# Kernel tuning notes

Hardware: AMD Instinct MI355X
Metric: run time of the kernel (lower is better)

Reference implementation:

```python
import jax, jax.numpy as jnp
import numpy as np

TEMPERATURE = 0.1
EPS = 1e-8


def _hann(T, dtype):
    # torch.hann_window default: periodic=True -> 0.5*(1-cos(2*pi*n/T))
    return 0.5 * (1.0 - jnp.cos(2.0 * jnp.pi * jnp.arange(T, dtype=dtype) / T))


def _per_traj_stats(trajectories):
    # trajectories: [B, T, 4] = (phi1, v1, phi2, v2)
    B, T, _ = trajectories.shape
    v = trajectories[:, :, 1::2]                      # [B, T, 2] voltages
    v_mean = v.mean(axis=1)                           # [B, 2]
    w = _hann(T, trajectories.dtype)[None, :, None]
    fft = jnp.fft.rfft(v * w, axis=1)                 # [B, T//2+1, 2]
    psd = (jnp.abs(fft) ** 2)[:, : T // 10, :]        # keep low-frequency bins
    psd = psd.reshape(B, -1)                          # [B, 2*(T//10)] (flatten, C-order like torch)
    phase = trajectories[:, :, 0::2]                  # [B, T, 2]
    delta = jnp.diff(phase, axis=1)
    winding = jnp.abs(jnp.round(delta.sum(axis=1) / (2.0 * jnp.pi)))  # [B, 2]
    return v_mean, psd, winding


def _kinematic_similarity(trajectories):
    # Vectorized equivalent of the original O(B^2) python loop (i < j, symmetrized, zero diag)
    v_mean, psd, winding = _per_traj_stats(trajectories)
    v_dist = jnp.linalg.norm(v_mean[:, None, :] - v_mean[None, :, :], axis=-1)  # [B, B]
    v_sim = jnp.exp(-v_dist / 0.5)
    n2 = jnp.sum(psd * psd, axis=1)                   # [B]
    gram = psd @ psd.T                                # [B, B]
    d2 = jnp.maximum(n2[:, None] + n2[None, :] - 2.0 * gram, 0.0)
    psd_dist = jnp.sqrt(d2)
    psd_norm = jnp.sqrt(n2)
    # denominator uses ||psd_i|| of the row index (matches loop where i < j)
    psd_sim = jnp.exp(-psd_dist / (psd_norm[:, None] + EPS))
    wind_sim = jnp.all(winding[:, None, :] == winding[None, :, :], axis=-1).astype(psd.dtype)
    total = 0.4 * v_sim + 0.4 * psd_sim + 0.2 * wind_sim
    upper = jnp.triu(total, k=1)                      # only i<j computed in the loop
    return upper + upper.T                            # symmetric, zero diagonal


def reference(features, labels, trajectories, param_scales):
    B = features.shape[0]
    # F.normalize(dim=1), eps=1e-12
    norm = jnp.maximum(jnp.linalg.norm(features, axis=1, keepdims=True), 1e-12)
    f = features / norm
    param_diff = jnp.abs(labels[:, None, :] - labels[None, :, :]) / param_scales
    param_dist = jnp.linalg.norm(param_diff, axis=2)  # [B, B]
    kin_sim = jax.lax.stop_gradient(_kinematic_similarity(trajectories))  # no_grad in torch
    mask_pos_weight = jnp.exp(-param_dist / 0.1) * kin_sim
    sim = (f @ f.T) / TEMPERATURE
    exp_sim = jnp.exp(sim)
    exp_sim = jnp.where(jnp.eye(B, dtype=bool), 0.0, exp_sim)
    pos_weighted = (exp_sim * mask_pos_weight).sum(axis=1)
    denom = exp_sim.sum(axis=1)
    loss = -jnp.log((pos_weighted + EPS) / (denom + EPS))
    return loss.mean()


def setup_inputs() -> dict:
    key = jax.random.key(0)
    k1, k2, k3 = jax.random.split(key, 3)
    B, D, T, P = 1024, 256, 8192, 3
    features = jax.random.normal(k1, (B, D), dtype=jnp.float32)
    labels = jax.random.uniform(k2, (B, P), dtype=jnp.float32)
    trajectories = jax.random.normal(k3, (B, T, 4), dtype=jnp.float32)
    param_scales = jnp.ones((1,), dtype=jnp.float32)
    return {"features": features, "labels": labels, "trajectories": trajectories, "param_scales": param_scales}
```

## Files before the change

### kernel.cpp

```cpp
#include <hip/hip_runtime.h>
#include <hip/hip_bf16.h>

#define B_SZ 1024
#define T_LEN 8192
#define NBINS 819
#define PSD_LDA 1664
#define PI_F 3.14159265358979323846f

typedef __attribute__((ext_vector_type(8))) short bf16x8;
typedef __attribute__((ext_vector_type(4))) float f32x4;

__device__ constexpr float W32C[32] = {
  1.0f, 0.980785280f, 0.923879533f, 0.831469612f, 0.707106781f, 0.555570233f,
  0.382683432f, 0.195090322f, 0.0f, -0.195090322f, -0.382683432f, -0.555570233f,
  -0.707106781f, -0.831469612f, -0.923879533f, -0.980785280f, -1.0f,
  -0.980785280f, -0.923879533f, -0.831469612f, -0.707106781f, -0.555570233f,
  -0.382683432f, -0.195090322f, 0.0f, 0.195090322f, 0.382683432f, 0.555570233f,
  0.707106781f, 0.831469612f, 0.923879533f, 0.980785280f};
__device__ constexpr float W32S[32] = {
  0.0f, -0.195090322f, -0.382683432f, -0.555570233f, -0.707106781f,
  -0.831469612f, -0.923879533f, -0.980785280f, -1.0f, -0.980785280f,
  -0.923879533f, -0.831469612f, -0.707106781f, -0.555570233f, -0.382683432f,
  -0.195090322f, 0.0f, 0.195090322f, 0.382683432f, 0.555570233f, 0.707106781f,
  0.831469612f, 0.923879533f, 0.980785280f, 1.0f, 0.980785280f, 0.923879533f,
  0.831469612f, 0.707106781f, 0.555570233f, 0.382683432f, 0.195090322f};
__device__ constexpr float E8C[8] = {
  1.0f, 0.707106781f, 0.0f, -0.707106781f, -1.0f, -0.707106781f, 0.0f, 0.707106781f};
__device__ constexpr float E8S[8] = {
  0.0f, 0.707106781f, 1.0f, 0.707106781f, 0.0f, -0.707106781f, -1.0f, -0.707106781f};

__device__ __forceinline__ unsigned short bfb(float x) {
  __hip_bfloat16 h = __float2bfloat16(x);
  return *(unsigned short*)&h;
}
__device__ __forceinline__ float bff(unsigned short u) {
  union { unsigned u; float f; } v; v.u = ((unsigned)u) << 16; return v.f;
}
__device__ __forceinline__ unsigned cvtpk(float r, float i) {
  unsigned out;
  asm("v_cvt_pk_bf16_f32 %0, %1, %2" : "=v"(out) : "v"(r), "v"(i));
  return out;
}
union U8 { bf16x8 v; unsigned u[4]; };

#define WIDX(k0, b, c) ((k0) * 288 + 9 * (b) + (c))

template<int K, int LDA>
__device__ __forceinline__ void gram_body(
    const __hip_bfloat16* __restrict__ A, float* __restrict__ C,
    int i0, int j0, int tid, void* ldsraw) {
  __hip_bfloat16 (*lds)[64][64] = (__hip_bfloat16 (*)[64][64])ldsraw;
  const int lane = tid & 63;
  const int wave = tid >> 6;
  const int wm = wave >> 1, wn = wave & 1;

  f32x4 acc[2][2] = {};

  for (int k0 = 0; k0 < K; k0 += 64) {
    #pragma unroll
    for (int r = 0; r < 2; ++r) {
      int e   = tid + 256 * r;
      int row = e >> 3;
      int cb  = e & 7;
      int scb = cb ^ (row & 7);
      const __hip_bfloat16* srcA = A + (size_t)(i0 + row) * LDA + k0 + scb * 8;
      const __hip_bfloat16* srcB = A + (size_t)(j0 + row) * LDA + k0 + scb * 8;
      __builtin_amdgcn_global_load_lds(
          (const __attribute__((address_space(1))) void*)srcA,
          (__attribute__((address_space(3))) void*)(&lds[0][0][0] + e * 8),
          16, 0, 0);
      __builtin_amdgcn_global_load_lds(
          (const __attribute__((address_space(1))) void*)srcB,
          (__attribute__((address_space(3))) void*)(&lds[1][0][0] + e * 8),
          16, 0, 0);
    }
    __syncthreads();

    #pragma unroll
    for (int ks = 0; ks < 2; ++ks) {
      bf16x8 afr[2], bfr[2];
      #pragma unroll
      for (int m = 0; m < 2; ++m) {
        int row = wm * 32 + m * 16 + (lane & 15);
        int cidx = ks * 4 + (lane >> 4);
        int cc  = cidx ^ (row & 7);
        afr[m] = *(const bf16x8*)(&lds[0][row][cc * 8]);
      }
      #pragma unroll
      for (int n = 0; n < 2; ++n) {
        int row = wn * 32 + n * 16 + (lane & 15);
        int cidx = ks * 4 + (lane >> 4);
        int cc  = cidx ^ (row & 7);
        bfr[n] = *(const bf16x8*)(&lds[1][row][cc * 8]);
      }
      #pragma unroll
      for (int m = 0; m < 2; ++m)
        #pragma unroll
        for (int n = 0; n < 2; ++n)
          acc[m][n] = __builtin_amdgcn_mfma_f32_16x16x32_bf16(
              afr[m], bfr[n], acc[m][n], 0, 0, 0);
    }
    __syncthreads();
  }

  #pragma unroll
  for (int m = 0; m < 2; ++m)
    #pragma unroll
    for (int n = 0; n < 2; ++n)
      #pragma unroll
      for (int r = 0; r < 4; ++r) {
        int row = i0 + wm * 32 + m * 16 + (lane >> 4) * 4 + r;
        int col = j0 + wn * 32 + n * 16 + (lane & 15);
        C[(size_t)row * B_SZ + col] = acc[m][n][r];
      }
}

__global__ __launch_bounds__(256) void normalize_kernel(
    const float* __restrict__ f, __hip_bfloat16* __restrict__ fn) {
  int i = blockIdx.x;
  int t = threadIdx.x;
  float v = f[(size_t)i * 256 + t];
  float s = v * v;
  #pragma unroll
  for (int o = 32; o; o >>= 1) s += __shfl_down(s, o);
  __shared__ float buf[4];
  if ((t & 63) == 0) buf[t >> 6] = s;
  __syncthreads();
  float norm = sqrtf(buf[0] + buf[1] + buf[2] + buf[3]);
  norm = fmaxf(norm, 1e-12f);
  fn[(size_t)i * 256 + t] = __float2bfloat16(v / norm);
}

__global__ __launch_bounds__(256) void traj_featgram_kernel(
    const float* __restrict__ trajf,
    __hip_bfloat16* __restrict__ psd,
    float2* __restrict__ vmean,
    float2* __restrict__ wind,
    const __hip_bfloat16* __restrict__ f_n,
    float* __restrict__ S) {
  __shared__ __align__(16) unsigned z2w[9216];
  __shared__ float rsum[2][4];
  __shared__ float phb[4];

  const int tid = threadIdx.x;

  if (blockIdx.x >= B_SZ) {
    const int e  = blockIdx.x - B_SZ;
    gram_body<256, 256>(f_n, S, (e >> 4) * 64, (e & 15) * 64, tid, (void*)z2w);
    return;
  }

  const int w   = tid >> 6;
  const int l   = tid & 63;
  const int g   = l >> 4;
  const int lc  = l & 15;
  const float* rowf = trajf + (size_t)blockIdx.x * T_LEN * 4;

  if (tid == 0) {
    phb[0] = rowf[0]; phb[1] = rowf[2];
    phb[2] = rowf[(size_t)4 * (T_LEN - 1)];
    phb[3] = rowf[(size_t)4 * (T_LEN - 1) + 2];
  }

  bf16x8 Ac[2], As[2], Asn[2];
  #pragma unroll
  for (int mt = 0; mt < 2; ++mt) {
    const int m = mt * 16 + lc;
    #pragma unroll
    for (int j = 0; j < 8; ++j) {
      const int idx = (m * (g * 8 + j)) & 31;
      unsigned short uc = bfb(W32C[idx]);
      unsigned short us = bfb(W32S[idx]);
      Ac[mt][j]  = (short)uc;
      As[mt][j]  = (short)us;
      Asn[mt][j] = (short)(us ^ 0x8000);
    }
  }

  float vs0 = 0.f, vs1 = 0.f;
  const f32x4 az = {0.f, 0.f, 0.f, 0.f};

  #pragma unroll
  for (int nt = 0; nt < 4; ++nt) {
    const int n = w * 64 + nt * 16 + lc;
    float yr[8], yw[8];
    #pragma unroll
    for (int j = 0; j < 8; ++j) {
      const size_t t = (size_t)(g * 8 + j) * 256 + n;
      yr[j] = rowf[4 * t + 1];
      yw[j] = rowf[4 * t + 3];
    }
    #pragma unroll
    for (int j = 0; j < 8; ++j) { vs0 += yr[j]; vs1 += yw[j]; }
    float s0, c0;
    __sincosf(2.0f * PI_F * ((float)n / 8192.0f + (float)g * 0.25f), &s0, &c0);
    U8 xrb, xib;
    #pragma unroll
    for (int j2 = 0; j2 < 4; ++j2) {
      float w0 = 0.5f - 0.5f * (c0 * W32C[2*j2]   + s0 * W32S[2*j2]);
      float w1 = 0.5f - 0.5f * (c0 * W32C[2*j2+1] + s0 * W32S[2*j2+1]);
      xrb.u[j2] = cvtpk(yr[2*j2] * w0, yr[2*j2+1] * w1);
      xib.u[j2] = cvtpk(yw[2*j2] * w0, yw[2*j2+1] * w1);
    }
    const int bw = 9 * (n >> 3) + (n & 7);
    float ss, cs;
    __sincosf(-2.0f * PI_F * (float)n / 8192.0f, &ss, &cs);
    #pragma unroll
    for (int mt = 0; mt < 2; ++mt) {
      f32x4 ar = __builtin_amdgcn_mfma_f32_16x16x32_bf16(Asn[mt], xib.v, az, 0, 0, 0);
      ar = __builtin_amdgcn_mfma_f32_16x16x32_bf16(Ac[mt], xrb.v, ar, 0, 0, 0);
      f32x4 ai = __builtin_amdgcn_mfma_f32_16x16x32_bf16(Ac[mt], xib.v, az, 0, 0, 0);
      ai = __builtin_amdgcn_mfma_f32_16x16x32_bf16(As[mt], xrb.v, ai, 0, 0, 0);
      float sb, cb;
      __sincosf(-2.0f * PI_F * (float)n * (float)(mt * 16 + g * 4) / 8192.0f, &sb, &cb);
      #pragma unroll
      for (int r = 0; r < 4; ++r) {
        float xr_ = ar[r] * cb - ai[r] * sb;
        float xi_ = ar[r] * sb + ai[r] * cb;
        const int k0 = mt * 16 + g * 4 + r;
        z2w[k0 * 288 + bw] = cvtpk(xr_, xi_);
        float nc = cb * cs - sb * ss; sb = cb * ss + sb * cs; cb = nc;
      }
    }
  }
  __syncthreads();

  unsigned x2_0[2][4], x2_1[2][4], x2_2[2][4], x2_3[2][4];
  #pragma unroll
  for (int nt = 0; nt < 4; ++nt) {
    const int n2 = w * 64 + nt * 16 + lc;
    const int k0 = n2 >> 3, cc = n2 & 7;
    U8 xrb, xib;
    #pragma unroll
    for (int j2 = 0; j2 < 4; ++j2) {
      unsigned p0 = z2w[WIDX(k0, g * 8 + 2*j2,     cc)];
      unsigned p1 = z2w[WIDX(k0, g * 8 + 2*j2 + 1, cc)];
      xrb.u[j2] = (p0 & 0xffffu) | (p1 << 16);
      xib.u[j2] = (p0 >> 16) | (p1 & 0xffff0000u);
    }
    #pragma unroll
    for (int mt = 0; mt < 2; ++mt) {
      f32x4 ar = __builtin_amdgcn_mfma_f32_16x16x32_bf16(Asn[mt], xib.v, az, 0, 0, 0);
      ar = __builtin_amdgcn_mfma_f32_16x16x32_bf16(Ac[mt], xrb.v, ar, 0, 0, 0);
      f32x4 ai = __builtin_amdgcn_mfma_f32_16x16x32_bf16(Ac[mt], xib.v, az, 0, 0, 0);
      ai = __builtin_amdgcn_mfma_f32_16x16x32_bf16(As[mt], xrb.v, ai, 0, 0, 0);
      float sb, cb, ss, cs;
      const float cf = (float)cc;
      __sincosf(-2.0f * PI_F * cf * (float)(mt * 16 + g * 4) / 256.0f, &sb, &cb);
      __sincosf(-2.0f * PI_F * cf / 256.0f, &ss, &cs);
      #pragma unroll
      for (int r = 0; r < 4; ++r) {
        float xr_ = ar[r] * cb - ai[r] * sb;
        float xi_ = ar[r] * sb + ai[r] * cb;
        unsigned pk = cvtpk(xr_, xi_);
        if (nt == 0) x2_0[mt][r] = pk;
        else if (nt == 1) x2_1[mt][r] = pk;
        else if (nt == 2) x2_2[mt][r] = pk;
        else x2_3[mt][r] = pk;
        float nc = cb * cs - sb * ss; sb = cb * ss + sb * cs; cb = nc;
      }
    }
  }
  __syncthreads();

  #pragma unroll
  for (int nt = 0; nt < 4; ++nt) {
    const int n2 = w * 64 + nt * 16 + lc;
    const int k0 = n2 >> 3, cc = n2 & 7;
    #pragma unroll
    for (int mt = 0; mt < 2; ++mt)
      #pragma unroll
      for (int r = 0; r < 4; ++r) {
        const int p = (mt * 16 + g * 4 + r) * 32 + k0;
        unsigned pk = (nt == 0) ? x2_0[mt][r] : (nt == 1) ? x2_1[mt][r]
                    : (nt == 2) ? x2_2[mt][r] : x2_3[mt][r];
        z2w[(p << 3) + (cc ^ ((p >> 2) & 7))] = pk;
      }
  }
  __syncthreads();

  float z0r[4], z0i[4], z7r[4], z7i[4];
  #pragma unroll
  for (int q = 0; q < 4; ++q) {
    const int p = q * 256 + tid;
    float s0r = 0.f, s0i = 0.f, s7r = 0.f, s7i = 0.f;
    #pragma unroll
    for (int c2 = 0; c2 < 8; ++c2) {
      unsigned pw = z2w[(p << 3) + (c2 ^ ((p >> 2) & 7))];
      float vr = bff((unsigned short)(pw & 0xffff));
      float vi = bff((unsigned short)(pw >> 16));
      s0r += vr; s0i += vi;
      s7r += vr * E8C[c2] - vi * E8S[c2];
      s7i += vr * E8S[c2] + vi * E8C[c2];
    }
    z0r[q] = s0r; z0i[q] = s0i; z7r[q] = s7r; z7i[q] = s7i;
  }
  __syncthreads();
  float2* zf = (float2*)z2w;
  #pragma unroll
  for (int q = 0; q < 4; ++q) {
    const int p = q * 256 + tid;
    zf[p]        = make_float2(z0r[q], z0i[q]);
    zf[1024 + p] = make_float2(z7r[q], z7i[q]);
  }
  __syncthreads();

  for (int k = tid; k < PSD_LDA / 2; k += 256) {
    if (k < NBINS) {
      float2 Zk = zf[k];
      float2 Zn = (k == 0) ? zf[0] : zf[2048 - k];
      float fxr = 0.5f * (Zk.x + Zn.x);
      float fxi = 0.5f * (Zk.y - Zn.y);
      float fyr = 0.5f * (Zk.y + Zn.y);
      float fyi = 0.5f * (Zn.x - Zk.x);
      psd[(size_t)blockIdx.x * PSD_LDA + 2*k]     = __float2bfloat16(fxr*fxr + fxi*fxi);
      psd[(size_t)blockIdx.x * PSD_LDA + 2*k + 1] = __float2bfloat16(fyr*fyr + fyi*fyi);
    } else {
      psd[(size_t)blockIdx.x * PSD_LDA + 2*k]     = __float2bfloat16(0.0f);
      psd[(size_t)blockIdx.x * PSD_LDA + 2*k + 1] = __float2bfloat16(0.0f);
    }
  }

  #pragma unroll
  for (int o = 32; o; o >>= 1) {
    vs0 += __shfl_down(vs0, o);
    vs1 += __shfl_down(vs1, o);
  }
  if ((tid & 63) == 0) { rsum[0][tid >> 6] = vs0; rsum[1][tid >> 6] = vs1; }
  __syncthreads();
  if (tid == 0) {
    float s0 = rsum[0][0] + rsum[0][1] + rsum[0][2] + rsum[0][3];
    float s1v = rsum[1][0] + rsum[1][1] + rsum[1][2] + rsum[1][3];
    vmean[blockIdx.x] = make_float2(s0 / (float)T_LEN, s1v / (float)T_LEN);
    const float inv2pi = 0.15915494309189535f;
    wind[blockIdx.x] = make_float2(fabsf(rintf((phb[2] - phb[0]) * inv2pi)),
                                   fabsf(rintf((phb[3] - phb[1]) * inv2pi)));
  }
}

template<int K, int LDA, int KOFF>
__global__ __launch_bounds__(256) void gram_mfma_kernel(
    const __hip_bfloat16* __restrict__ A, float* __restrict__ C) {
  __shared__ __align__(16) __hip_bfloat16 lds[2][64][64];
  gram_body<K, LDA>(A + (size_t)blockIdx.z * KOFF,
                    C + (size_t)blockIdx.z * B_SZ * B_SZ,
                    blockIdx.y * 64, blockIdx.x * 64, threadIdx.x, (void*)lds);
}

__global__ __launch_bounds__(256) void loss_rows_kernel(
    const float* __restrict__ S,
    const float* __restrict__ G,
    const float* __restrict__ labels,
    const float* __restrict__ scales,
    const float2* __restrict__ vmean,
    const float2* __restrict__ wind,
    float* __restrict__ row_loss) {
  const int i = blockIdx.x;
  const int tid = threadIdx.x;
  const float* G2 = G + (size_t)B_SZ * B_SZ;
  const float inv_scale = 1.0f / scales[0];
  const float l0 = labels[i*3+0], l1 = labels[i*3+1], l2 = labels[i*3+2];
  const float2 vmi = vmean[i];
  const float2 wi  = wind[i];
  const float n2i  = G[(size_t)i * B_SZ + i] + G2[(size_t)i * B_SZ + i];
  const float normi = sqrtf(n2i);

  float posw = 0.f, den = 0.f;
  for (int j = tid; j < B_SZ; j += 256) {
    if (j == i) continue;
    float e = __expf(S[(size_t)i * B_SZ + j] * 10.0f);
    den += e;

    float d0 = (labels[j*3+0] - l0) * inv_scale;
    float d1 = (labels[j*3+1] - l1) * inv_scale;
    float d2v = (labels[j*3+2] - l2) * inv_scale;
    float pd = sqrtf(d0*d0 + d1*d1 + d2v*d2v);
    float pw = __expf(-pd * 10.0f);

    float2 vmj = vmean[j];
    float dvx = vmi.x - vmj.x, dvy = vmi.y - vmj.y;
    float v_sim = __expf(-sqrtf(dvx*dvx + dvy*dvy) * 2.0f);

    float n2j = G[(size_t)j * B_SZ + j] + G2[(size_t)j * B_SZ + j];
    float gg  = G[(size_t)i * B_SZ + j] + G2[(size_t)i * B_SZ + j];
    float dd  = fmaxf(n2i + n2j - 2.0f * gg, 0.0f);
    float psd_dist = sqrtf(dd);
    float norma = (i < j) ? normi : sqrtf(n2j);
    float psd_sim = __expf(-psd_dist / (norma + 1e-8f));

    float2 wj = wind[j];
    float w_sim = (wi.x == wj.x && wi.y == wj.y) ? 1.0f : 0.0f;

    float kin = 0.4f * v_sim + 0.4f * psd_sim + 0.2f * w_sim;
    posw += e * pw * kin;
  }

  #pragma unroll
  for (int o = 32; o; o >>= 1) {
    posw += __shfl_down(posw, o);
    den  += __shfl_down(den, o);
  }
  __shared__ float bp[4], bd[4];
  if ((tid & 63) == 0) { bp[tid >> 6] = posw; bd[tid >> 6] = den; }
  __syncthreads();
  if (tid == 0) {
    float P = bp[0] + bp[1] + bp[2] + bp[3];
    float D = bd[0] + bd[1] + bd[2] + bd[3];
    row_loss[i] = -logf((P + 1e-8f) / (D + 1e-8f));
  }
}

__global__ __launch_bounds__(256) void reduce_mean_kernel(
    const float* __restrict__ row_loss, float* __restrict__ out) {
  int tid = threadIdx.x;
  float s = 0.f;
  for (int i = tid; i < B_SZ; i += 256) s += row_loss[i];
  #pragma unroll
  for (int o = 32; o; o >>= 1) s += __shfl_down(s, o);
  __shared__ float buf[4];
  if ((tid & 63) == 0) buf[tid >> 6] = s;
  __syncthreads();
  if (tid == 0) out[0] = (buf[0] + buf[1] + buf[2] + buf[3]) / (float)B_SZ;
}

extern "C" void kernel_launch(void* const* d_in, const int* in_sizes, int n_in,
                              void* d_out, int out_size, void* d_ws, size_t ws_size,
                              hipStream_t stream) {
  const float* features = (const float*)d_in[0];
  const float* labels   = (const float*)d_in[1];
  const float* traj     = (const float*)d_in[2];
  const float* scales   = (const float*)d_in[3];

  char* ws = (char*)d_ws;
  __hip_bfloat16* f_n = (__hip_bfloat16*)ws;
  __hip_bfloat16* psd = (__hip_bfloat16*)(ws + (size_t)B_SZ*256*2);
  float* G = (float*)(ws + (size_t)B_SZ*256*2 + (size_t)B_SZ*PSD_LDA*2);
  float* S = G + 2 * (size_t)B_SZ * B_SZ;
  float2* vmean = (float2*)(S + (size_t)B_SZ * B_SZ);
  float2* wind  = vmean + B_SZ;
  float* row_loss = (float*)(wind + B_SZ);

  normalize_kernel<<<B_SZ, 256, 0, stream>>>(features, f_n);
  traj_featgram_kernel<<<B_SZ + 256, 256, 0, stream>>>(
      traj, psd, vmean, wind, f_n, S);

  dim3 gridPsd(16, 16, 2);
  gram_mfma_kernel<832, PSD_LDA, 832><<<gridPsd, 256, 0, stream>>>(psd, G);

  loss_rows_kernel<<<B_SZ, 256, 0, stream>>>(S, G, labels, scales, vmean, wind, row_loss);
  reduce_mean_kernel<<<1, 256, 0, stream>>>(row_loss, (float*)d_out);
}
```

Before: 63.02 us.

## Fuse feature normalization into gram blocks and split PSD gram into four K-slices

Removes the separate normalize kernel: the feature-gram blocks now compute row inverse norms themselves and convert the fp32 features to normalized bf16 while staging them into LDS. The PSD gram split-K goes from 2 to 4 slices (K=448 each, with the PSD row stride padded to 1792) to expose more blocks, and the loss kernel sums four partial grams. This saves one launch and the f_n round trip, but gram blocks now do redundant norm work and synchronous loads instead of async global-to-LDS copies, and the loss kernel reads twice as much G data.

Result: slower. 68.12 us (+8.1%).

```diff
diff --git a/kernel.cpp b/kernel.cpp
--- a/kernel.cpp
+++ b/kernel.cpp
@@ -4,7 +4,7 @@
 #define B_SZ 1024
 #define T_LEN 8192
 #define NBINS 819
-#define PSD_LDA 1664
+#define PSD_LDA 1792
 #define PI_F 3.14159265358979323846f
 
 typedef __attribute__((ext_vector_type(8))) short bf16x8;
@@ -45,17 +45,61 @@
 
 #define WIDX(k0, b, c) ((k0) * 288 + 9 * (b) + (c))
 
+__device__ __forceinline__ void gram_mfma_step(
+    void* ldsraw, int tid, f32x4 (&acc)[2][2]) {
+  __hip_bfloat16 (*lds)[64][64] = (__hip_bfloat16 (*)[64][64])ldsraw;
+  const int lane = tid & 63;
+  const int wave = tid >> 6;
+  const int wm = wave >> 1, wn = wave & 1;
+  #pragma unroll
+  for (int ks = 0; ks < 2; ++ks) {
+    bf16x8 afr[2], bfr[2];
+    #pragma unroll
+    for (int m = 0; m < 2; ++m) {
+      int row = wm * 32 + m * 16 + (lane & 15);
+      int cidx = ks * 4 + (lane >> 4);
+      int cc  = cidx ^ (row & 7);
+      afr[m] = *(const bf16x8*)(&lds[0][row][cc * 8]);
+    }
+    #pragma unroll
+    for (int n = 0; n < 2; ++n) {
+      int row = wn * 32 + n * 16 + (lane & 15);
+      int cidx = ks * 4 + (lane >> 4);
+      int cc  = cidx ^ (row & 7);
+      bfr[n] = *(const bf16x8*)(&lds[1][row][cc * 8]);
+    }
+    #pragma unroll
+    for (int m = 0; m < 2; ++m)
+      #pragma unroll
+      for (int n = 0; n < 2; ++n)
+        acc[m][n] = __builtin_amdgcn_mfma_f32_16x16x32_bf16(
+            afr[m], bfr[n], acc[m][n], 0, 0, 0);
+  }
+}
+
+__device__ __forceinline__ void gram_writeback(
+    float* __restrict__ C, int i0, int j0, int tid, f32x4 (&acc)[2][2]) {
+  const int lane = tid & 63;
+  const int wave = tid >> 6;
+  const int wm = wave >> 1, wn = wave & 1;
+  #pragma unroll
+  for (int m = 0; m < 2; ++m)
+    #pragma unroll
+    for (int n = 0; n < 2; ++n)
+      #pragma unroll
+      for (int r = 0; r < 4; ++r) {
+        int row = i0 + wm * 32 + m * 16 + (lane >> 4) * 4 + r;
+        int col = j0 + wn * 32 + n * 16 + (lane & 15);
+        C[(size_t)row * B_SZ + col] = acc[m][n][r];
+      }
+}
+
 template<int K, int LDA>
 __device__ __forceinline__ void gram_body(
     const __hip_bfloat16* __restrict__ A, float* __restrict__ C,
     int i0, int j0, int tid, void* ldsraw) {
   __hip_bfloat16 (*lds)[64][64] = (__hip_bfloat16 (*)[64][64])ldsraw;
-  const int lane = tid & 63;
-  const int wave = tid >> 6;
-  const int wm = wave >> 1, wn = wave & 1;
-
   f32x4 acc[2][2] = {};
-
   for (int k0 = 0; k0 < K; k0 += 64) {
     #pragma unroll
     for (int r = 0; r < 2; ++r) {
@@ -75,60 +119,65 @@
           16, 0, 0);
     }
     __syncthreads();
-
-    #pragma unroll
-    for (int ks = 0; ks < 2; ++ks) {
-      bf16x8 afr[2], bfr[2];
-      #pragma unroll
-      for (int m = 0; m < 2; ++m) {
-        int row = wm * 32 + m * 16 + (lane & 15);
-        int cidx = ks * 4 + (lane >> 4);
-        int cc  = cidx ^ (row & 7);
-        afr[m] = *(const bf16x8*)(&lds[0][row][cc * 8]);
+    gram_mfma_step(ldsraw, tid, acc);
+    __syncthreads();
+  }
+  gram_writeback(C, i0, j0, tid, acc);
+}
+
+__device__ __forceinline__ void featgram_body(
+    const float* __restrict__ feat, float* __restrict__ S,
+    int i0, int j0, int tid, void* ldsraw) {
+  __hip_bfloat16 (*lds)[64][64] = (__hip_bfloat16 (*)[64][64])ldsraw;
+  float* norm_inv = (float*)((char*)ldsraw + 2 * 64 * 64 * 2);
+
+  {
+    const int r = tid >> 1, h = tid & 1;
+    const int grow = (r < 64) ? (i0 + r) : (j0 + r - 64);
+    const float4* p = (const float4*)(feat + (size_t)grow * 256 + h * 128);
+    float s = 0.f;
+    #pragma unroll 8
+    for (int q = 0; q < 32; ++q) {
+      float4 v = p[q];
+      s += v.x * v.x + v.y * v.y + v.z * v.z + v.w * v.w;
+    }
+    s += __shfl_xor(s, 1);
+    if (h == 0) norm_inv[r] = 1.0f / fmaxf(sqrtf(s), 1e-12f);
+  }
+  __syncthreads();
+
+  f32x4 acc[2][2] = {};
+  for (int k0 = 0; k0 < 256; k0 += 64) {
+    #pragma unroll
+    for (int r = 0; r < 2; ++r) {
+      int e   = tid + 256 * r;
+      int row = e >> 3;
+      int cb  = e & 7;
+      int scb = cb ^ (row & 7);
+      {
+        const float* src = feat + (size_t)(i0 + row) * 256 + k0 + scb * 8;
+        float ni = norm_inv[row];
+        U8 pk;
+        #pragma unroll
+        for (int q = 0; q < 4; ++q)
+          pk.u[q] = cvtpk(src[2*q] * ni, src[2*q+1] * ni);
+        *(bf16x8*)(&lds[0][0][0] + e * 8) = pk.v;
       }
-      #pragma unroll
-      for (int n = 0; n < 2; ++n) {
-        int row = wn * 32 + n * 16 + (lane & 15);
-        int cidx = ks * 4 + (lane >> 4);
-        int cc  = cidx ^ (row & 7);
-        bfr[n] = *(const bf16x8*)(&lds[1][row][cc * 8]);
+      {
+        const float* src = feat + (size_t)(j0 + row) * 256 + k0 + scb * 8;
+        float ni = norm_inv[64 + row];
+        U8 pk;
+        #pragma unroll
+        for (int q = 0; q < 4; ++q)
+          pk.u[q] = cvtpk(src[2*q] * ni, src[2*q+1] * ni);
+        *(bf16x8*)(&lds[1][0][0] + e * 8) = pk.v;
       }
-      #pragma unroll
-      for (int m = 0; m < 2; ++m)
-        #pragma unroll
-        for (int n = 0; n < 2; ++n)
-          acc[m][n] = __builtin_amdgcn_mfma_f32_16x16x32_bf16(
-              afr[m], bfr[n], acc[m][n], 0, 0, 0);
     }
     __syncthreads();
-  }
-
-  #pragma unroll
-  for (int m = 0; m < 2; ++m)
-    #pragma unroll
-    for (int n = 0; n < 2; ++n)
-      #pragma unroll
-      for (int r = 0; r < 4; ++r) {
-        int row = i0 + wm * 32 + m * 16 + (lane >> 4) * 4 + r;
-        int col = j0 + wn * 32 + n * 16 + (lane & 15);
-        C[(size_t)row * B_SZ + col] = acc[m][n][r];
-      }
-}
-
-__global__ __launch_bounds__(256) void normalize_kernel(
-    const float* __restrict__ f, __hip_bfloat16* __restrict__ fn) {
-  int i = blockIdx.x;
-  int t = threadIdx.x;
-  float v = f[(size_t)i * 256 + t];
-  float s = v * v;
-  #pragma unroll
-  for (int o = 32; o; o >>= 1) s += __shfl_down(s, o);
-  __shared__ float buf[4];
-  if ((t & 63) == 0) buf[t >> 6] = s;
-  __syncthreads();
-  float norm = sqrtf(buf[0] + buf[1] + buf[2] + buf[3]);
-  norm = fmaxf(norm, 1e-12f);
-  fn[(size_t)i * 256 + t] = __float2bfloat16(v / norm);
+    gram_mfma_step(ldsraw, tid, acc);
+    __syncthreads();
+  }
+  gram_writeback(S, i0, j0, tid, acc);
 }
 
 __global__ __launch_bounds__(256) void traj_featgram_kernel(
@@ -136,7 +185,7 @@
     __hip_bfloat16* __restrict__ psd,
     float2* __restrict__ vmean,
     float2* __restrict__ wind,
-    const __hip_bfloat16* __restrict__ f_n,
+    const float* __restrict__ features,
     float* __restrict__ S) {
   __shared__ __align__(16) unsigned z2w[9216];
   __shared__ float rsum[2][4];
@@ -145,8 +194,8 @@
   const int tid = threadIdx.x;
 
   if (blockIdx.x >= B_SZ) {
-    const int e  = blockIdx.x - B_SZ;
-    gram_body<256, 256>(f_n, S, (e >> 4) * 64, (e & 15) * 64, tid, (void*)z2w);
+    const int e = blockIdx.x - B_SZ;
+    featgram_body(features, S, (e >> 4) * 64, (e & 15) * 64, tid, (void*)z2w);
     return;
   }
 
@@ -357,12 +406,13 @@
     float* __restrict__ row_loss) {
   const int i = blockIdx.x;
   const int tid = threadIdx.x;
-  const float* G2 = G + (size_t)B_SZ * B_SZ;
+  const size_t BB = (size_t)B_SZ * B_SZ;
   const float inv_scale = 1.0f / scales[0];
   const float l0 = labels[i*3+0], l1 = labels[i*3+1], l2 = labels[i*3+2];
   const float2 vmi = vmean[i];
   const float2 wi  = wind[i];
-  const float n2i  = G[(size_t)i * B_SZ + i] + G2[(size_t)i * B_SZ + i];
+  const float n2i = G[(size_t)i * B_SZ + i] + G[BB + (size_t)i * B_SZ + i]
+                  + G[2*BB + (size_t)i * B_SZ + i] + G[3*BB + (size_t)i * B_SZ + i];
   const float normi = sqrtf(n2i);
 
   float posw = 0.f, den = 0.f;
@@ -381,8 +431,10 @@
     float dvx = vmi.x - vmj.x, dvy = vmi.y - vmj.y;
     float v_sim = __expf(-sqrtf(dvx*dvx + dvy*dvy) * 2.0f);
 
-    float n2j = G[(size_t)j * B_SZ + j] + G2[(size_t)j * B_SZ + j];
-    float gg  = G[(size_t)i * B_SZ + j] + G2[(size_t)i * B_SZ + j];
+    float n2j = G[(size_t)j * B_SZ + j] + G[BB + (size_t)j * B_SZ + j]
+              + G[2*BB + (size_t)j * B_SZ + j] + G[3*BB + (size_t)j * B_SZ + j];
+    float gg  = G[(size_t)i * B_SZ + j] + G[BB + (size_t)i * B_SZ + j]
+              + G[2*BB + (size_t)i * B_SZ + j] + G[3*BB + (size_t)i * B_SZ + j];
     float dd  = fmaxf(n2i + n2j - 2.0f * gg, 0.0f);
     float psd_dist = sqrtf(dd);
     float norma = (i < j) ? normi : sqrtf(n2j);
@@ -432,20 +484,18 @@
   const float* scales   = (const float*)d_in[3];
 
   char* ws = (char*)d_ws;
-  __hip_bfloat16* f_n = (__hip_bfloat16*)ws;
-  __hip_bfloat16* psd = (__hip_bfloat16*)(ws + (size_t)B_SZ*256*2);
-  float* G = (float*)(ws + (size_t)B_SZ*256*2 + (size_t)B_SZ*PSD_LDA*2);
-  float* S = G + 2 * (size_t)B_SZ * B_SZ;
+  __hip_bfloat16* psd = (__hip_bfloat16*)ws;
+  float* G = (float*)(ws + (size_t)B_SZ * PSD_LDA * 2);
+  float* S = G + 4 * (size_t)B_SZ * B_SZ;
   float2* vmean = (float2*)(S + (size_t)B_SZ * B_SZ);
   float2* wind  = vmean + B_SZ;
   float* row_loss = (float*)(wind + B_SZ);
 
-  normalize_kernel<<<B_SZ, 256, 0, stream>>>(features, f_n);
   traj_featgram_kernel<<<B_SZ + 256, 256, 0, stream>>>(
-      traj, psd, vmean, wind, f_n, S);
-
-  dim3 gridPsd(16, 16, 2);
-  gram_mfma_kernel<832, PSD_LDA, 832><<<gridPsd, 256, 0, stream>>>(psd, G);
+      traj, psd, vmean, wind, features, S);
+
+  dim3 gridPsd(16, 16, 4);
+  gram_mfma_kernel<448, PSD_LDA, 448><<<gridPsd, 256, 0, stream>>>(psd, G);
 
   loss_rows_kernel<<<B_SZ, 256, 0, stream>>>(S, G, labels, scales, vmean, wind, row_loss);
   reduce_mean_kernel<<<1, 256, 0, stream>>>(row_loss, (float*)d_out);
```
